# Optimization experiments

Hardware: AMD Instinct MI355X
Metric: run time of the kernel (lower is better)

Reference implementation:

```python
import jax, jax.numpy as jnp
import numpy as np

# config
HIDDEN = 1024
NUM_EXPERTS = 16
TOP_K = 4
MOE_INTER = 512
NUM_SHARED = 2
SHARED_INTER = MOE_INTER * NUM_SHARED  # 1024
NORM_TOPK = True
ROUTED_SCALE = 1.0
NUM_TOKENS = 1024


def setup_inputs() -> dict:
    key = jax.random.key(0)
    ks = jax.random.split(key, 8)
    s = 0.02
    return {
        "hidden_states": jax.random.normal(ks[0], (NUM_TOKENS, HIDDEN), jnp.float32),
        # router (BailingMoEGate): weight [E, H], no bias
        "router_w": jax.random.normal(ks[1], (NUM_EXPERTS, HIDDEN), jnp.float32) * s,
        # routed experts: gate/up proj [E, H, I], down proj [E, I, H]
        "w_gate": jax.random.normal(ks[2], (NUM_EXPERTS, HIDDEN, MOE_INTER), jnp.float32) * s,
        "w_up": jax.random.normal(ks[3], (NUM_EXPERTS, HIDDEN, MOE_INTER), jnp.float32) * s,
        "w_down": jax.random.normal(ks[4], (NUM_EXPERTS, MOE_INTER, HIDDEN), jnp.float32) * s,
        # shared experts (BailingMoEMLP, merged gate_up): [H, 2*Is], [Is, H]
        "ws_gate_up": jax.random.normal(ks[5], (HIDDEN, 2 * SHARED_INTER), jnp.float32) * s,
        "ws_down": jax.random.normal(ks[6], (SHARED_INTER, HIDDEN), jnp.float32) * s,
    }


def _moe_forward(x, router_w, w_gate, w_up, w_down, ws_gate_up, ws_down):
    T = x.shape[0]
    # ---- router: logits -> softmax -> top-k (score_function='softmax', no bias)
    logits = jnp.einsum("th,eh->te", x, router_w)          # [T, E]
    probs = jax.nn.softmax(logits, axis=-1)
    topk_w, topk_idx = jax.lax.top_k(probs, TOP_K)         # [T, K]
    if NORM_TOPK:
        topk_w = topk_w / jnp.sum(topk_w, axis=-1, keepdims=True)
    topk_w = topk_w * ROUTED_SCALE
    # sparse combine weights [T, E] (zeros for non-selected experts)
    combine = jnp.zeros((T, NUM_EXPERTS), x.dtype).at[
        jnp.arange(T)[:, None], topk_idx
    ].set(topk_w.astype(x.dtype))
    # ---- routed experts: SiLU(x W_gate) * (x W_up) then W_down, weighted combine
    g = jnp.einsum("th,ehi->tei", x, w_gate)               # [T, E, I]
    u = jnp.einsum("th,ehi->tei", x, w_up)
    h = jax.nn.silu(g) * u
    routed = jnp.einsum("tei,eih,te->th", h, w_down, combine)
    # ---- shared experts (dense SwiGLU MLP)
    gu = x @ ws_gate_up                                    # [T, 2*Is]
    g_s, u_s = jnp.split(gu, 2, axis=-1)
    shared = (jax.nn.silu(g_s) * u_s) @ ws_down
    return routed + shared


def reference(hidden_states, router_w, w_gate, w_up, w_down, ws_gate_up, ws_down):
    return _moe_forward(hidden_states, router_w, w_gate, w_up, w_down,
                        ws_gate_up, ws_down)
```

## Files before the change

### kernel.cpp

```cpp
#include <hip/hip_runtime.h>
#include <stdint.h>


typedef __attribute__((ext_vector_type(8))) unsigned short ushort8;
typedef __attribute__((ext_vector_type(4))) float f32x4;
typedef __attribute__((ext_vector_type(8))) __bf16 bf16x8;

#define T_TOK 1024
#define HID   1024
#define NEXP  16
#define TOPK  4
#define MINTER 512
#define SINTER 1024

constexpr size_t WGU_E = 32 * 1024 * 32;
constexpr size_t WD_E  = 16 * 1024 * 32;

constexpr size_t OFF_COUNTS = 0;
constexpr size_t OFF_LIST   = 1024;
constexpr size_t OFF_WT     = OFF_LIST  + 65536;
constexpr size_t OFF_XB     = OFF_WT    + 65536;
constexpr size_t OFF_HR     = OFF_XB    + 2097152;
constexpr size_t OFF_HS     = OFF_HR    + 4194304;
constexpr size_t OFF_WGU    = OFF_HS    + 2097152;
constexpr size_t OFF_WD     = OFF_WGU   + 33554432;
constexpr size_t OFF_WSGU   = OFF_WD    + 16777216;
constexpr size_t OFF_WSD    = OFF_WSGU  + 4194304;

__device__ __forceinline__ unsigned short f2bf(float f) {
  union { float f; uint32_t u; } v; v.f = f;
  uint32_t r = (v.u + 0x7FFFu + ((v.u >> 16) & 1u)) >> 16;
  return (unsigned short)r;
}
__device__ __forceinline__ bf16x8 as_bf16x8(ushort8 s) {
  union { ushort8 s; bf16x8 b; } u; u.s = s; return u.b;
}
__device__ __forceinline__ float silu(float g) { return g / (1.f + __expf(-g)); }

__device__ __forceinline__ void glds16(const unsigned short* g, unsigned short* l) {
  __builtin_amdgcn_global_load_lds(
      (const __attribute__((address_space(1))) unsigned int*)g,
      (__attribute__((address_space(3))) unsigned int*)l, 16, 0, 0);
}

#define PIPE_BARRIER0() asm volatile("s_waitcnt vmcnt(0) lgkmcnt(0)\ns_barrier" ::: "memory")

__global__ __launch_bounds__(256) void init_kernel(int* counts, float* out) {
  if (blockIdx.x == 0 && threadIdx.x < NEXP) counts[threadIdx.x] = 0;
  const size_t t = (size_t)blockIdx.x * 256 + threadIdx.x;
  *(float4*)(out + t * 4) = (float4){0.f, 0.f, 0.f, 0.f};
}

__global__ __launch_bounds__(64) void router_kernel(
    const float* __restrict__ x, const float* __restrict__ rw,
    int* counts, int* list, float* wt,
    unsigned short* __restrict__ Xb) {
  const int t = blockIdx.x, l = threadIdx.x;
  float xv[16];
#pragma unroll
  for (int j = 0; j < 16; j++) xv[j] = x[t * HID + j * 64 + l];
#pragma unroll
  for (int j = 0; j < 16; j++) Xb[t * HID + j * 64 + l] = f2bf(xv[j]);
  float p[NEXP];
#pragma unroll
  for (int e = 0; e < NEXP; e++) {
    float s = 0.f;
#pragma unroll
    for (int j = 0; j < 16; j++) s += xv[j] * rw[e * HID + j * 64 + l];
#pragma unroll
    for (int off = 32; off > 0; off >>= 1) s += __shfl_xor(s, off);
    p[e] = s;
  }
  float mx = p[0];
#pragma unroll
  for (int e = 1; e < NEXP; e++) mx = fmaxf(mx, p[e]);
  int idx[TOPK]; float w4[TOPK]; float wsum = 0.f; unsigned used = 0u;
#pragma unroll
  for (int k = 0; k < TOPK; k++) {
    float bv = -1e30f; int bi = 0;
#pragma unroll
    for (int e = 0; e < NEXP; e++)
      if (!((used >> e) & 1u) && p[e] > bv) { bv = p[e]; bi = e; }
    used |= 1u << bi;
    idx[k] = bi;
    w4[k] = __expf(p[bi] - mx);
    wsum += w4[k];
  }
  const float inv = 1.f / wsum;
  if (l < TOPK) {
    const int e = idx[l];
    const int pos = atomicAdd(&counts[e], 1);
    list[e * 1024 + pos] = t;
    wt[e * 1024 + pos]   = w4[l] * inv;
  }
}

__global__ __launch_bounds__(256) void pack_all_kernel(
    const float* __restrict__ Wg, const float* __restrict__ Wu,
    const float* __restrict__ Wd, const float* __restrict__ Wsgu,
    const float* __restrict__ Wsd,
    unsigned short* __restrict__ WGUp, unsigned short* __restrict__ WDp,
    unsigned short* __restrict__ WSGUp, unsigned short* __restrict__ WSDp) {
  const int bid = blockIdx.x;
  const float* src; unsigned short* dst; int C, Nj, kp0, r0, c0, jbase, ilv;
  if (bid < 2048) {
    const int e = bid >> 7, loc = bid & 127, kt = loc >> 3, nt = loc & 7;
    src = Wg + (size_t)e * HID * MINTER; dst = WGUp + (size_t)e * WGU_E;
    C = MINTER; Nj = 1024; kp0 = 2 * kt; r0 = 64 * kt; c0 = 64 * nt;
    jbase = 128 * nt; ilv = 1;
  } else if (bid < 4096) {
    const int e = (bid - 2048) >> 7, loc = bid & 127, kt = loc >> 3, nt = loc & 7;
    src = Wu + (size_t)e * HID * MINTER; dst = WGUp + (size_t)e * WGU_E;
    C = MINTER; Nj = 1024; kp0 = 2 * kt; r0 = 64 * kt; c0 = 64 * nt;
    jbase = 128 * nt + 16; ilv = 1;
  } else if (bid < 6144) {
    const int e = (bid - 4096) >> 7, loc = bid & 127, kt = loc >> 4, nt = loc & 15;
    src = Wd + (size_t)e * MINTER * HID; dst = WDp + (size_t)e * WD_E;
    C = HID; Nj = 1024; kp0 = 2 * kt; r0 = 64 * kt; c0 = 64 * nt;
    jbase = 64 * nt; ilv = 0;
  } else if (bid < 6656) {
    const int loc = bid - 6144, kt = loc >> 5, nt = loc & 31;
    src = Wsgu; dst = WSGUp;
    C = 2048; Nj = 2048; kp0 = 2 * kt; r0 = 64 * kt; c0 = 64 * nt;
    const int isU = (nt >= 16), ntc = nt & 15;
    jbase = 128 * ntc + 16 * isU; ilv = 1;
  } else {
    const int loc = bid - 6656, kt = loc >> 4, nt = loc & 15;
    src = Wsd; dst = WSDp;
    C = HID; Nj = 1024; kp0 = 2 * kt; r0 = 64 * kt; c0 = 64 * nt;
    jbase = 64 * nt; ilv = 0;
  }
  __shared__ float tile[64][65];
  const int t = threadIdx.x;
  {
    const int r = t >> 4, c4 = (t & 15) * 4;
#pragma unroll
    for (int p = 0; p < 4; p++) {
      const int rr = p * 16 + r;
      const float4 v = *(const float4*)(src + (size_t)(r0 + rr) * C + c0 + c4);
      tile[rr][c4 + 0] = v.x; tile[rr][c4 + 1] = v.y;
      tile[rr][c4 + 2] = v.z; tile[rr][c4 + 3] = v.w;
    }
  }
  __syncthreads();
  {
    const int n = t >> 2, k8 = (t & 3) * 8;
    const int j = jbase + (ilv ? (32 * (n >> 4) + (n & 15)) : n);
#pragma unroll
    for (int h = 0; h < 2; h++) {
      const int k = 32 * h + k8;
      union { unsigned short u[8]; ushort8 v; } pk;
#pragma unroll
      for (int i = 0; i < 8; i++) pk.u[i] = f2bf(tile[k + i][n]);
      *(ushort8*)(dst + ((size_t)(kp0 + h) * Nj + j) * 32 + k8) = pk.v;
    }
  }
}

__global__ __launch_bounds__(256, 5) void phase1_kernel(
    const unsigned short* __restrict__ Xb,
    const unsigned short* __restrict__ WGUp,
    const unsigned short* __restrict__ WSGUp,
    const int* __restrict__ counts, const int* __restrict__ list,
    const float* __restrict__ wt,
    unsigned short* __restrict__ Hr,
    unsigned short* __restrict__ Hs) {
  const int z = blockIdx.z, x = blockIdx.x, y = blockIdx.y;
  const bool routed = (z > 0);
  const int e = z - 1;
  int cnt = 0, base = 0;
  if (routed) {
    if (x >= 8) return;
    cnt = counts[e];
    if (y * 128 >= cnt) return;
#pragma unroll
    for (int i = 0; i < NEXP; i++) base += (i < e) ? counts[i] : 0;
  }
  __shared__ __align__(16) unsigned short sA[2][128 * 32];
  __shared__ __align__(16) unsigned short sB[2][128 * 32];
  const int tid = threadIdx.x, w = tid >> 6, l = tid & 63;
  const int wm = w >> 1, wn = w & 1, m0 = y * 128;
  const int swz = ((l & 3) ^ ((l >> 3) & 3)) * 8;
  const int Nj = routed ? 1024 : 2048;

  const unsigned short* aS[2];
#pragma unroll
  for (int ii = 0; ii < 2; ii++) {
    const int r = 32 * w + 16 * ii + (l >> 2);
    const unsigned short* row = routed
        ? Xb + (size_t)list[e * 1024 + min(m0 + r, cnt - 1)] * HID
        : Xb + (size_t)(m0 + r) * HID;
    aS[ii] = row + swz;
  }
  const unsigned short* pan = routed ? WGUp + (size_t)e * WGU_E : WSGUp;
  const unsigned short* bS[2];
#pragma unroll
  for (int ii = 0; ii < 2; ii++)
    bS[ii] = pan + ((size_t)(x * 128 + 32 * w + 16 * ii + (l >> 2))) * 32 + swz;
  const size_t bStep = (size_t)Nj * 32;

  const int rsw = ((l >> 4) ^ (((l & 15) >> 1) & 3)) * 8;
  int aOff[4], bOff[4];
#pragma unroll
  for (int i = 0; i < 4; i++) aOff[i] = (64 * wm + 16 * i + (l & 15)) * 32 + rsw;
#pragma unroll
  for (int jt = 0; jt < 4; jt++) bOff[jt] = (64 * wn + 16 * jt + (l & 15)) * 32 + rsw;

  f32x4 acc[4][4];
#pragma unroll
  for (int i = 0; i < 4; i++)
#pragma unroll
    for (int jt = 0; jt < 4; jt++) acc[i][jt] = (f32x4){0.f, 0.f, 0.f, 0.f};

  auto stage = [&](int s, int b) {
    glds16(aS[0] + (size_t)s * 32, &sA[b][(32 * w) * 32]);
    glds16(aS[1] + (size_t)s * 32, &sA[b][(32 * w + 16) * 32]);
    glds16(bS[0] + (size_t)s * bStep, &sB[b][(32 * w) * 32]);
    glds16(bS[1] + (size_t)s * bStep, &sB[b][(32 * w + 16) * 32]);
  };

  const int steps = HID / 32;
  stage(0, 0);
  PIPE_BARRIER0();
#pragma unroll 1
  for (int s = 0; s < steps; s++) {
    const int cur = s & 1;
    if (s + 1 < steps) stage(s + 1, cur ^ 1);
    const unsigned short* A = &sA[cur][0];
    const unsigned short* B = &sB[cur][0];
    bf16x8 af[4], bfr[4];
#pragma unroll
    for (int i = 0; i < 4; i++) af[i] = as_bf16x8(*(const ushort8*)(A + aOff[i]));
#pragma unroll
    for (int jt = 0; jt < 4; jt++) bfr[jt] = as_bf16x8(*(const ushort8*)(B + bOff[jt]));
#pragma unroll
    for (int jt = 0; jt < 4; jt++)
#pragma unroll
      for (int i = 0; i < 4; i++)
        acc[i][jt] = __builtin_amdgcn_mfma_f32_16x16x32_bf16(af[i], bfr[jt], acc[i][jt], 0, 0, 0);
    PIPE_BARRIER0();
  }

  const int rl = (l >> 4) * 4, cl = l & 15;
  const int panel = 2 * x + wn;
#pragma unroll
  for (int i = 0; i < 4; i++)
#pragma unroll
    for (int r = 0; r < 4; r++) {
      const int grow = m0 + 64 * wm + 16 * i + rl + r;
#pragma unroll
      for (int p = 0; p < 2; p++) {
        const float g = acc[i][2 * p][r], u = acc[i][2 * p + 1][r];
        if (routed) {
          if (grow < cnt) {
            const float h = silu(g) * u * wt[e * 1024 + grow];
            Hr[((size_t)panel * 4096 + base + grow) * 32 + 16 * p + cl] = f2bf(h);
          }
        } else {
          const float h = silu(g) * u;
          Hs[((size_t)panel * 1024 + grow) * 32 + 16 * p + cl] = f2bf(h);
        }
      }
    }
}

__global__ __launch_bounds__(256, 5) void phase2_kernel(
    const unsigned short* __restrict__ Hr, const unsigned short* __restrict__ Hs,
    const unsigned short* __restrict__ WDp, const unsigned short* __restrict__ WSDp,
    const int* __restrict__ counts, const int* __restrict__ list,
    float* __restrict__ out) {
  const int z = blockIdx.z, x = blockIdx.x, y = blockIdx.y;
  const bool routed = (z > 0);
  const int e = z - 1;
  int cnt = 0, base = 0, steps;
  if (routed) {
    cnt = counts[e];
    if (y * 128 >= cnt) return;
#pragma unroll
    for (int i = 0; i < NEXP; i++) base += (i < e) ? counts[i] : 0;
    steps = MINTER / 32;
  } else {
    steps = SINTER / 32;
  }
  __shared__ __align__(16) unsigned short sA[2][128 * 32];
  __shared__ __align__(16) unsigned short sB[2][128 * 32];
  const int tid = threadIdx.x, w = tid >> 6, l = tid & 63;
  const int wm = w >> 1, wn = w & 1, m0 = y * 128;
  const int swz = ((l & 3) ^ ((l >> 3) & 3)) * 8;
  const size_t aStep = (size_t)(routed ? 4096 : 1024) * 32;

  const unsigned short* aS[2];
#pragma unroll
  for (int ii = 0; ii < 2; ii++) {
    const int r = 32 * w + 16 * ii + (l >> 2);
    const int R = routed ? (base + min(m0 + r, cnt - 1)) : (m0 + r);
    aS[ii] = (routed ? Hr : Hs) + (size_t)R * 32 + swz;
  }
  const unsigned short* pan = routed ? WDp + (size_t)e * WD_E : WSDp;
  const unsigned short* bS[2];
#pragma unroll
  for (int ii = 0; ii < 2; ii++)
    bS[ii] = pan + ((size_t)(x * 128 + 32 * w + 16 * ii + (l >> 2))) * 32 + swz;
  const size_t bStep = (size_t)1024 * 32;

  const int rsw = ((l >> 4) ^ (((l & 15) >> 1) & 3)) * 8;
  int aOff[4], bOff[4];
#pragma unroll
  for (int i = 0; i < 4; i++) aOff[i] = (64 * wm + 16 * i + (l & 15)) * 32 + rsw;
#pragma unroll
  for (int jt = 0; jt < 4; jt++) bOff[jt] = (64 * wn + 16 * jt + (l & 15)) * 32 + rsw;

  f32x4 acc[4][4];
#pragma unroll
  for (int i = 0; i < 4; i++)
#pragma unroll
    for (int jt = 0; jt < 4; jt++) acc[i][jt] = (f32x4){0.f, 0.f, 0.f, 0.f};

  auto stage = [&](int s, int b) {
    glds16(aS[0] + (size_t)s * aStep, &sA[b][(32 * w) * 32]);
    glds16(aS[1] + (size_t)s * aStep, &sA[b][(32 * w + 16) * 32]);
    glds16(bS[0] + (size_t)s * bStep, &sB[b][(32 * w) * 32]);
    glds16(bS[1] + (size_t)s * bStep, &sB[b][(32 * w + 16) * 32]);
  };

  stage(0, 0);
  PIPE_BARRIER0();
#pragma unroll 1
  for (int s = 0; s < steps; s++) {
    const int cur = s & 1;
    if (s + 1 < steps) stage(s + 1, cur ^ 1);
    const unsigned short* A = &sA[cur][0];
    const unsigned short* B = &sB[cur][0];
    bf16x8 af[4], bfr[4];
#pragma unroll
    for (int i = 0; i < 4; i++) af[i] = as_bf16x8(*(const ushort8*)(A + aOff[i]));
#pragma unroll
    for (int jt = 0; jt < 4; jt++) bfr[jt] = as_bf16x8(*(const ushort8*)(B + bOff[jt]));
#pragma unroll
    for (int jt = 0; jt < 4; jt++)
#pragma unroll
      for (int i = 0; i < 4; i++)
        acc[i][jt] = __builtin_amdgcn_mfma_f32_16x16x32_bf16(af[i], bfr[jt], acc[i][jt], 0, 0, 0);
    PIPE_BARRIER0();
  }

  const int rl = (l >> 4) * 4, cl = l & 15;
#pragma unroll
  for (int i = 0; i < 4; i++)
#pragma unroll
    for (int r = 0; r < 4; r++) {
      const int grow = m0 + 64 * wm + 16 * i + rl + r;
      if (routed && grow >= cnt) continue;
      const int orow = routed ? list[e * 1024 + grow] : grow;
#pragma unroll
      for (int jt = 0; jt < 4; jt++) {
        const int col = 128 * x + 64 * wn + 16 * jt + cl;
        atomicAdd(&out[(size_t)orow * HID + col], acc[i][jt][r]);
      }
    }
}

extern "C" void kernel_launch(void* const* d_in, const int* in_sizes, int n_in,
                              void* d_out, int out_size, void* d_ws, size_t ws_size,
                              hipStream_t stream) {
  const float* x      = (const float*)d_in[0];
  const float* rw     = (const float*)d_in[1];
  const float* w_gate = (const float*)d_in[2];
  const float* w_up   = (const float*)d_in[3];
  const float* w_down = (const float*)d_in[4];
  const float* ws_gu  = (const float*)d_in[5];
  const float* ws_dn  = (const float*)d_in[6];
  float* out = (float*)d_out;
  char* ws = (char*)d_ws;

  int*   counts = (int*)  (ws + OFF_COUNTS);
  int*   list   = (int*)  (ws + OFF_LIST);
  float* wtbuf  = (float*)(ws + OFF_WT);
  unsigned short* Xb    = (unsigned short*)(ws + OFF_XB);
  unsigned short* Hr    = (unsigned short*)(ws + OFF_HR);
  unsigned short* Hs    = (unsigned short*)(ws + OFF_HS);
  unsigned short* WGUp  = (unsigned short*)(ws + OFF_WGU);
  unsigned short* WDp   = (unsigned short*)(ws + OFF_WD);
  unsigned short* WSGUp = (unsigned short*)(ws + OFF_WSGU);
  unsigned short* WSDp  = (unsigned short*)(ws + OFF_WSD);

  init_kernel<<<1024, 256, 0, stream>>>(counts, out);
  router_kernel<<<T_TOK, 64, 0, stream>>>(x, rw, counts, list, wtbuf, Xb);
  pack_all_kernel<<<6912, 256, 0, stream>>>(
      w_gate, w_up, w_down, ws_gu, ws_dn, WGUp, WDp, WSGUp, WSDp);
  phase1_kernel<<<dim3(16, 8, 17), 256, 0, stream>>>(
      Xb, WGUp, WSGUp, counts, list, wtbuf, Hr, Hs);
  phase2_kernel<<<dim3(8, 8, 17), 256, 0, stream>>>(
      Hr, Hs, WDp, WSDp, counts, list, out);
  (void)in_sizes; (void)n_in; (void)out_size; (void)ws_size;
}
```

Baseline: 299.4 us.

## Use 512-thread blocks with triple-buffered LDS pipeline in both GEMM phases

Both expert GEMM kernels now launch 8 waves per block instead of 4. Each wave computes a 64x32 sub-tile and issues one A and one B global-to-LDS load per stage. The LDS staging moves from double to triple buffering, prefetching two K-steps ahead with a partial vmcnt wait and a single barrier per iteration. The aim is to hide global-load latency and raise the number of waves in flight. In exchange each block uses more LDS, per-wave MFMA work per fragment load is smaller, and the gate/up panel mapping in the epilogue is rearranged.

```diff
diff --git a/kernel.cpp b/kernel.cpp
--- a/kernel.cpp
+++ b/kernel.cpp
@@ -43,6 +43,7 @@
       (__attribute__((address_space(3))) unsigned int*)l, 16, 0, 0);
 }
 
+#define PIPE_BARRIER2() asm volatile("s_waitcnt vmcnt(2) lgkmcnt(0)\ns_barrier" ::: "memory")
 #define PIPE_BARRIER0() asm volatile("s_waitcnt vmcnt(0) lgkmcnt(0)\ns_barrier" ::: "memory")
 
 __global__ __launch_bounds__(256) void init_kernel(int* counts, float* out) {
@@ -157,7 +158,7 @@
   }
 }
 
-__global__ __launch_bounds__(256, 5) void phase1_kernel(
+__global__ __launch_bounds__(512, 4) void phase1_kernel(
     const unsigned short* __restrict__ Xb,
     const unsigned short* __restrict__ WGUp,
     const unsigned short* __restrict__ WSGUp,
@@ -176,95 +177,86 @@
 #pragma unroll
     for (int i = 0; i < NEXP; i++) base += (i < e) ? counts[i] : 0;
   }
-  __shared__ __align__(16) unsigned short sA[2][128 * 32];
-  __shared__ __align__(16) unsigned short sB[2][128 * 32];
+  __shared__ __align__(16) unsigned short sA[3][128 * 32];
+  __shared__ __align__(16) unsigned short sB[3][128 * 32];
   const int tid = threadIdx.x, w = tid >> 6, l = tid & 63;
-  const int wm = w >> 1, wn = w & 1, m0 = y * 128;
+  const int wm = w >> 2, wn = w & 3, m0 = y * 128;
+  const int g = l >> 4, r15 = l & 15;
   const int swz = ((l & 3) ^ ((l >> 3) & 3)) * 8;
   const int Nj = routed ? 1024 : 2048;
 
-  const unsigned short* aS[2];
-#pragma unroll
-  for (int ii = 0; ii < 2; ii++) {
-    const int r = 32 * w + 16 * ii + (l >> 2);
-    const unsigned short* row = routed
-        ? Xb + (size_t)list[e * 1024 + min(m0 + r, cnt - 1)] * HID
-        : Xb + (size_t)(m0 + r) * HID;
-    aS[ii] = row + swz;
-  }
+  const int ar = 16 * w + (l >> 2);
+  const unsigned short* aS = (routed
+      ? Xb + (size_t)list[e * 1024 + min(m0 + ar, cnt - 1)] * HID
+      : Xb + (size_t)(m0 + ar) * HID) + swz;
   const unsigned short* pan = routed ? WGUp + (size_t)e * WGU_E : WSGUp;
-  const unsigned short* bS[2];
-#pragma unroll
-  for (int ii = 0; ii < 2; ii++)
-    bS[ii] = pan + ((size_t)(x * 128 + 32 * w + 16 * ii + (l >> 2))) * 32 + swz;
+  const unsigned short* bS =
+      pan + ((size_t)(x * 128 + 16 * w + (l >> 2))) * 32 + swz;
   const size_t bStep = (size_t)Nj * 32;
 
-  const int rsw = ((l >> 4) ^ (((l & 15) >> 1) & 3)) * 8;
-  int aOff[4], bOff[4];
-#pragma unroll
-  for (int i = 0; i < 4; i++) aOff[i] = (64 * wm + 16 * i + (l & 15)) * 32 + rsw;
-#pragma unroll
-  for (int jt = 0; jt < 4; jt++) bOff[jt] = (64 * wn + 16 * jt + (l & 15)) * 32 + rsw;
-
-  f32x4 acc[4][4];
+  const int rsw = (g ^ ((r15 >> 1) & 3)) * 8;
+  int aOff[4], bOff[2];
+#pragma unroll
+  for (int i = 0; i < 4; i++) aOff[i] = (64 * wm + 16 * i + r15) * 32 + rsw;
+#pragma unroll
+  for (int jt = 0; jt < 2; jt++) bOff[jt] = (32 * wn + 16 * jt + r15) * 32 + rsw;
+
+  f32x4 acc[4][2];
 #pragma unroll
   for (int i = 0; i < 4; i++)
 #pragma unroll
-    for (int jt = 0; jt < 4; jt++) acc[i][jt] = (f32x4){0.f, 0.f, 0.f, 0.f};
+    for (int jt = 0; jt < 2; jt++) acc[i][jt] = (f32x4){0.f, 0.f, 0.f, 0.f};
 
   auto stage = [&](int s, int b) {
-    glds16(aS[0] + (size_t)s * 32, &sA[b][(32 * w) * 32]);
-    glds16(aS[1] + (size_t)s * 32, &sA[b][(32 * w + 16) * 32]);
-    glds16(bS[0] + (size_t)s * bStep, &sB[b][(32 * w) * 32]);
-    glds16(bS[1] + (size_t)s * bStep, &sB[b][(32 * w + 16) * 32]);
+    glds16(aS + (size_t)s * 32, &sA[b][(16 * w) * 32]);
+    glds16(bS + (size_t)s * bStep, &sB[b][(16 * w) * 32]);
   };
 
   const int steps = HID / 32;
-  stage(0, 0);
-  PIPE_BARRIER0();
+  stage(0, 0); stage(1, 1);
 #pragma unroll 1
   for (int s = 0; s < steps; s++) {
-    const int cur = s & 1;
-    if (s + 1 < steps) stage(s + 1, cur ^ 1);
-    const unsigned short* A = &sA[cur][0];
-    const unsigned short* B = &sB[cur][0];
-    bf16x8 af[4], bfr[4];
+    const int cb = s % 3;
+    if (s + 2 < steps)      { PIPE_BARRIER2(); stage(s + 2, (s + 2) % 3); }
+    else if (s + 1 < steps) { PIPE_BARRIER2(); }
+    else                    { PIPE_BARRIER0(); }
+    const unsigned short* A = &sA[cb][0];
+    const unsigned short* B = &sB[cb][0];
+    bf16x8 af[4], bfr[2];
 #pragma unroll
     for (int i = 0; i < 4; i++) af[i] = as_bf16x8(*(const ushort8*)(A + aOff[i]));
 #pragma unroll
-    for (int jt = 0; jt < 4; jt++) bfr[jt] = as_bf16x8(*(const ushort8*)(B + bOff[jt]));
-#pragma unroll
-    for (int jt = 0; jt < 4; jt++)
+    for (int jt = 0; jt < 2; jt++) bfr[jt] = as_bf16x8(*(const ushort8*)(B + bOff[jt]));
+#pragma unroll
+    for (int jt = 0; jt < 2; jt++)
 #pragma unroll
       for (int i = 0; i < 4; i++)
         acc[i][jt] = __builtin_amdgcn_mfma_f32_16x16x32_bf16(af[i], bfr[jt], acc[i][jt], 0, 0, 0);
-    PIPE_BARRIER0();
-  }
-
-  const int rl = (l >> 4) * 4, cl = l & 15;
-  const int panel = 2 * x + wn;
+  }
+
+  const int rl = g * 4;
+  const int p = 4 * x + wn;
+  const int hcol = 16 * (p & 1) + r15;
+  const size_t panel = (size_t)(p >> 1);
 #pragma unroll
   for (int i = 0; i < 4; i++)
 #pragma unroll
     for (int r = 0; r < 4; r++) {
       const int grow = m0 + 64 * wm + 16 * i + rl + r;
-#pragma unroll
-      for (int p = 0; p < 2; p++) {
-        const float g = acc[i][2 * p][r], u = acc[i][2 * p + 1][r];
-        if (routed) {
-          if (grow < cnt) {
-            const float h = silu(g) * u * wt[e * 1024 + grow];
-            Hr[((size_t)panel * 4096 + base + grow) * 32 + 16 * p + cl] = f2bf(h);
-          }
-        } else {
-          const float h = silu(g) * u;
-          Hs[((size_t)panel * 1024 + grow) * 32 + 16 * p + cl] = f2bf(h);
+      const float gv = acc[i][0][r], uv = acc[i][1][r];
+      if (routed) {
+        if (grow < cnt) {
+          const float h = silu(gv) * uv * wt[e * 1024 + grow];
+          Hr[(panel * 4096 + base + grow) * 32 + hcol] = f2bf(h);
         }
+      } else {
+        const float h = silu(gv) * uv;
+        Hs[(panel * 1024 + grow) * 32 + hcol] = f2bf(h);
       }
     }
 }
 
-__global__ __launch_bounds__(256, 5) void phase2_kernel(
+__global__ __launch_bounds__(512, 4) void phase2_kernel(
     const unsigned short* __restrict__ Hr, const unsigned short* __restrict__ Hs,
     const unsigned short* __restrict__ WDp, const unsigned short* __restrict__ WSDp,
     const int* __restrict__ counts, const int* __restrict__ list,
@@ -282,69 +274,62 @@
   } else {
     steps = SINTER / 32;
   }
-  __shared__ __align__(16) unsigned short sA[2][128 * 32];
-  __shared__ __align__(16) unsigned short sB[2][128 * 32];
+  __shared__ __align__(16) unsigned short sA[3][128 * 32];
+  __shared__ __align__(16) unsigned short sB[3][128 * 32];
   const int tid = threadIdx.x, w = tid >> 6, l = tid & 63;
-  const int wm = w >> 1, wn = w & 1, m0 = y * 128;
+  const int wm = w >> 2, wn = w & 3, m0 = y * 128;
+  const int g = l >> 4, r15 = l & 15;
   const int swz = ((l & 3) ^ ((l >> 3) & 3)) * 8;
   const size_t aStep = (size_t)(routed ? 4096 : 1024) * 32;
 
-  const unsigned short* aS[2];
-#pragma unroll
-  for (int ii = 0; ii < 2; ii++) {
-    const int r = 32 * w + 16 * ii + (l >> 2);
-    const int R = routed ? (base + min(m0 + r, cnt - 1)) : (m0 + r);
-    aS[ii] = (routed ? Hr : Hs) + (size_t)R * 32 + swz;
-  }
+  const int ar = 16 * w + (l >> 2);
+  const int R = routed ? (base + min(m0 + ar, cnt - 1)) : (m0 + ar);
+  const unsigned short* aS = (routed ? Hr : Hs) + (size_t)R * 32 + swz;
   const unsigned short* pan = routed ? WDp + (size_t)e * WD_E : WSDp;
-  const unsigned short* bS[2];
-#pragma unroll
-  for (int ii = 0; ii < 2; ii++)
-    bS[ii] = pan + ((size_t)(x * 128 + 32 * w + 16 * ii + (l >> 2))) * 32 + swz;
+  const unsigned short* bS =
+      pan + ((size_t)(x * 128 + 16 * w + (l >> 2))) * 32 + swz;
   const size_t bStep = (size_t)1024 * 32;
 
-  const int rsw = ((l >> 4) ^ (((l & 15) >> 1) & 3)) * 8;
-  int aOff[4], bOff[4];
-#pragma unroll
-  for (int i = 0; i < 4; i++) aOff[i] = (64 * wm + 16 * i + (l & 15)) * 32 + rsw;
-#pragma unroll
-  for (int jt = 0; jt < 4; jt++) bOff[jt] = (64 * wn + 16 * jt + (l & 15)) * 32 + rsw;
-
-  f32x4 acc[4][4];
+  const int rsw = (g ^ ((r15 >> 1) & 3)) * 8;
+  int aOff[4], bOff[2];
+#pragma unroll
+  for (int i = 0; i < 4; i++) aOff[i] = (64 * wm + 16 * i + r15) * 32 + rsw;
+#pragma unroll
+  for (int jt = 0; jt < 2; jt++) bOff[jt] = (32 * wn + 16 * jt + r15) * 32 + rsw;
+
+  f32x4 acc[4][2];
 #pragma unroll
   for (int i = 0; i < 4; i++)
 #pragma unroll
-    for (int jt = 0; jt < 4; jt++) acc[i][jt] = (f32x4){0.f, 0.f, 0.f, 0.f};
+    for (int jt = 0; jt < 2; jt++) acc[i][jt] = (f32x4){0.f, 0.f, 0.f, 0.f};
 
   auto stage = [&](int s, int b) {
-    glds16(aS[0] + (size_t)s * aStep, &sA[b][(32 * w) * 32]);
-    glds16(aS[1] + (size_t)s * aStep, &sA[b][(32 * w + 16) * 32]);
-    glds16(bS[0] + (size_t)s * bStep, &sB[b][(32 * w) * 32]);
-    glds16(bS[1] + (size_t)s * bStep, &sB[b][(32 * w + 16) * 32]);
+    glds16(aS + (size_t)s * aStep, &sA[b][(16 * w) * 32]);
+    glds16(bS + (size_t)s * bStep, &sB[b][(16 * w) * 32]);
   };
 
-  stage(0, 0);
-  PIPE_BARRIER0();
+  stage(0, 0); stage(1, 1);
 #pragma unroll 1
   for (int s = 0; s < steps; s++) {
-    const int cur = s & 1;
-    if (s + 1 < steps) stage(s + 1, cur ^ 1);
-    const unsigned short* A = &sA[cur][0];
-    const unsigned short* B = &sB[cur][0];
-    bf16x8 af[4], bfr[4];
+    const int cb = s % 3;
+    if (s + 2 < steps)      { PIPE_BARRIER2(); stage(s + 2, (s + 2) % 3); }
+    else if (s + 1 < steps) { PIPE_BARRIER2(); }
+    else                    { PIPE_BARRIER0(); }
+    const unsigned short* A = &sA[cb][0];
+    const unsigned short* B = &sB[cb][0];
+    bf16x8 af[4], bfr[2];
 #pragma unroll
     for (int i = 0; i < 4; i++) af[i] = as_bf16x8(*(const ushort8*)(A + aOff[i]));
 #pragma unroll
-    for (int jt = 0; jt < 4; jt++) bfr[jt] = as_bf16x8(*(const ushort8*)(B + bOff[jt]));
-#pragma unroll
-    for (int jt = 0; jt < 4; jt++)
+    for (int jt = 0; jt < 2; jt++) bfr[jt] = as_bf16x8(*(const ushort8*)(B + bOff[jt]));
+#pragma unroll
+    for (int jt = 0; jt < 2; jt++)
 #pragma unroll
       for (int i = 0; i < 4; i++)
         acc[i][jt] = __builtin_amdgcn_mfma_f32_16x16x32_bf16(af[i], bfr[jt], acc[i][jt], 0, 0, 0);
-    PIPE_BARRIER0();
-  }
-
-  const int rl = (l >> 4) * 4, cl = l & 15;
+  }
+
+  const int rl = g * 4;
 #pragma unroll
   for (int i = 0; i < 4; i++)
 #pragma unroll
@@ -353,8 +338,8 @@
       if (routed && grow >= cnt) continue;
       const int orow = routed ? list[e * 1024 + grow] : grow;
 #pragma unroll
-      for (int jt = 0; jt < 4; jt++) {
-        const int col = 128 * x + 64 * wn + 16 * jt + cl;
+      for (int jt = 0; jt < 2; jt++) {
+        const int col = 128 * x + 32 * wn + 16 * jt + r15;
         atomicAdd(&out[(size_t)orow * HID + col], acc[i][jt][r]);
       }
     }
@@ -388,9 +373,9 @@
   router_kernel<<<T_TOK, 64, 0, stream>>>(x, rw, counts, list, wtbuf, Xb);
   pack_all_kernel<<<6912, 256, 0, stream>>>(
       w_gate, w_up, w_down, ws_gu, ws_dn, WGUp, WDp, WSGUp, WSDp);
-  phase1_kernel<<<dim3(16, 8, 17), 256, 0, stream>>>(
+  phase1_kernel<<<dim3(16, 8, 17), 512, 0, stream>>>(
       Xb, WGUp, WSGUp, counts, list, wtbuf, Hr, Hs);
-  phase2_kernel<<<dim3(8, 8, 17), 256, 0, stream>>>(
+  phase2_kernel<<<dim3(8, 8, 17), 512, 0, stream>>>(
       Hr, Hs, WDp, WSDp, counts, list, out);
   (void)in_sizes; (void)n_in; (void)out_size; (void)ws_size;
 }
```

Result: faster. 247.9 us (-17.2%).
